# Performance work log

Measured on AMD Instinct MI355X. Metric: run time of the kernel, lower is better.

Reference implementation:

```python
import jax, jax.numpy as jnp
import numpy as np

B, S_SRC, S_TRG = 128, 512, 128
VIN, VOUT = 128, 128
E, H = 128, 256          # embed, encoder hidden
HD = 2 * H               # decoder hidden = 512 (concat of bi-dir encoder states)
DENC = 2 * H             # encoder output feature dim = 512


def setup_inputs() -> dict:
    key = jax.random.key(0)
    ks = jax.random.split(key, 20)
    g = lambda k, shape: (jax.random.normal(k, shape, jnp.float32) * 0.05)
    inp = {
        "src": jax.random.randint(ks[0], (B, S_SRC), 0, VIN, jnp.int32),
        "trg": jax.random.randint(ks[1], (B, S_TRG), 0, VOUT, jnp.int32),
        # encoder
        "enc_emb": g(ks[2], (VIN, E)),
        "enc_Wih_f": g(ks[3], (4 * H, E)),
        "enc_Whh_f": g(ks[4], (4 * H, H)),
        "enc_b_f": g(ks[5], (4 * H,)),
        "enc_Wih_b": g(ks[6], (4 * H, E)),
        "enc_Whh_b": g(ks[7], (4 * H, H)),
        "enc_b_b": g(ks[8], (4 * H,)),
        # decoder
        "dec_emb": g(ks[9], (VOUT, E)),
        "dec_Wih": g(ks[10], (4 * HD, E + DENC)),
        "dec_Whh": g(ks[11], (4 * HD, HD)),
        "dec_b": g(ks[12], (4 * HD,)),
        # attention: Linear(dec_hid + enc_dim -> HD), v: Linear(HD -> 1)
        "attn_W": g(ks[13], (HD + DENC, HD)),
        "attn_b": g(ks[14], (HD,)),
        "attn_v": g(ks[15], (HD,)),
        # output projection
        "out_W": g(ks[16], (HD, VOUT)),
        "out_b": g(ks[17], (VOUT,)),
    }
    return inp


def _lstm_cell(h, c, x, Wih, Whh, b):
    gates = x @ Wih.T + h @ Whh.T + b               # [B, 4H]
    i, f, gg, o = jnp.split(gates, 4, axis=-1)       # PyTorch gate order i,f,g,o
    i, f, o = jax.nn.sigmoid(i), jax.nn.sigmoid(f), jax.nn.sigmoid(o)
    c = f * c + i * jnp.tanh(gg)
    h = o * jnp.tanh(c)
    return h, c


def _lstm_scan(xs, Wih, Whh, b, reverse=False):
    # xs: [S, B, E] -> hs: [S, B, H] (time-aligned), plus final (h, c)
    Bn, Hn = xs.shape[1], Whh.shape[1]
    init = (jnp.zeros((Bn, Hn), xs.dtype), jnp.zeros((Bn, Hn), xs.dtype))
    def step(carry, x):
        h, c = _lstm_cell(carry[0], carry[1], x, Wih, Whh, b)
        return (h, c), h
    (h, c), hs = jax.lax.scan(step, init, xs, reverse=reverse)
    return hs, h, c


def reference(src, trg, enc_emb, enc_Wih_f, enc_Whh_f, enc_b_f,
              enc_Wih_b, enc_Whh_b, enc_b_b, dec_emb, dec_Wih, dec_Whh,
              dec_b, attn_W, attn_b, attn_v, out_W, out_b):
    # ----- encoder (bidirectional LSTM) -----
    emb = enc_emb[src]                                # [B, S, E]
    xs = jnp.swapaxes(emb, 0, 1)                      # [S, B, E]
    hs_f, hf, cf = _lstm_scan(xs, enc_Wih_f, enc_Whh_f, enc_b_f, reverse=False)
    hs_b, hb, cb = _lstm_scan(xs, enc_Wih_b, enc_Whh_b, enc_b_b, reverse=True)
    enc_out = jnp.swapaxes(jnp.concatenate([hs_f, hs_b], -1), 0, 1)  # [B, S, 2H]
    hidden = jnp.concatenate([hf, hb], -1)            # [B, HD]  (hidden.view(1,B,-1))
    cell = jnp.concatenate([cf, cb], -1)              # [B, HD]

    # attention linear split: energy = tanh([h, enc] @ W + b)
    Wh, We = attn_W[:HD], attn_W[HD:]
    enc_proj = jnp.einsum("bsd,de->bse", enc_out, We)  # [B, S, HD] precomputed

    def dec_step(carry, tok):
        h, c = carry
        e = jnp.tanh(h[:, None, :] @ Wh + enc_proj + attn_b)     # [B, S, HD]
        scores = jnp.einsum("bse,e->bs", e, attn_v)              # [B, S]
        aw = jax.nn.softmax(scores, axis=1)
        ctx = jnp.einsum("bs,bsd->bd", aw, enc_out)              # [B, DENC]
        x = jnp.concatenate([dec_emb[tok], ctx], -1)             # [B, E+DENC]
        h, c = _lstm_cell(h, c, x, dec_Wih, dec_Whh, dec_b)
        logits = h @ out_W + out_b                               # [B, VOUT]
        return (h, c), logits

    # teacher forcing (ratio=1.0): input at step t is trg[:, t-1], t = 1..T-1
    toks = jnp.swapaxes(trg[:, :-1], 0, 1)            # [T-1, B]
    _, logits = jax.lax.scan(dec_step, (hidden, cell), toks)
    logits = jnp.swapaxes(logits, 0, 1)               # [B, T-1, VOUT]
    outputs = jnp.concatenate(
        [jnp.zeros((src.shape[0], 1, VOUT), logits.dtype), logits], axis=1)
    return outputs
```

## Files before the change

kernel.cpp:

```cpp
#include <hip/hip_runtime.h>


typedef _Float16 f16;
typedef _Float16 half8 __attribute__((ext_vector_type(8)));
typedef float f32x4 __attribute__((ext_vector_type(4)));
typedef char char8v __attribute__((ext_vector_type(8)));

#define MFMA16(a, b, c) __builtin_amdgcn_mfma_f32_16x16x32_f16((a), (b), (c), 0, 0, 0)

#define PSCALE (2.5f / 127.f)
#define PINV   (127.f / 2.5f)

__device__ __forceinline__ float fsig(float x) {
    return __builtin_amdgcn_rcpf(1.f + __expf(-x));
}
__device__ __forceinline__ float ftanh(float x) {
    return 1.f - 2.f * __builtin_amdgcn_rcpf(1.f + __expf(2.f * x));
}
__device__ __forceinline__ int frag_idx(int m, int k, int KS) {
    return (((m >> 4) * KS + (k >> 5)) * 64 + (((k >> 3) & 3) * 16 + (m & 15))) * 8 + (k & 7);
}

__device__ __forceinline__ void lds_barrier() {
    asm volatile("s_waitcnt lgkmcnt(0)" ::: "memory");
    __builtin_amdgcn_sched_barrier(0);
    __builtin_amdgcn_s_barrier();
    __builtin_amdgcn_sched_barrier(0);
}

__global__ void k_zero(unsigned* __restrict__ s)
{
    for (int z = threadIdx.x; z < 4112; z += 256) s[z] = 0u;
}

__global__ __launch_bounds__(256) void k_prep(
    const float* __restrict__ attn_W, const float* __restrict__ out_W,
    const float* __restrict__ enc_emb,
    const float* __restrict__ wihf, const float* __restrict__ wihb,
    const float* __restrict__ whhf, const float* __restrict__ whhb,
    const float* __restrict__ dec_emb, const float* __restrict__ dec_wih,
    const float* __restrict__ dec_whh,
    f16* __restrict__ WhT_sw, f16* __restrict__ outWT_sw,
    f16* __restrict__ whhf_sw, f16* __restrict__ whhb_sw,
    f16* __restrict__ decwih_sw, f16* __restrict__ decwhh_sw,
    f16* __restrict__ WeT, f16* __restrict__ emb16,
    f16* __restrict__ wihf16, f16* __restrict__ wihb16,
    f16* __restrict__ decemb16, float* __restrict__ out)
{
    long i = (long)blockIdx.x * 256 + threadIdx.x;
    if (i >= 3784704L) return;
    long idx = i;
    if (idx < 262144) {
        int j = idx & 7, lane = (idx >> 3) & 63, c = lane & 15, q = lane >> 4;
        int ks = (idx >> 9) & 15, nt = idx >> 13;
        WhT_sw[idx] = (f16)attn_W[(ks * 32 + q * 8 + j) * 512 + nt * 16 + c];
        return;
    }
    idx -= 262144;
    if (idx < 65536) {
        int j = idx & 7, lane = (idx >> 3) & 63, c = lane & 15, q = lane >> 4;
        int ks = (idx >> 9) & 15, nt = idx >> 13;
        outWT_sw[idx] = (f16)out_W[(ks * 32 + q * 8 + j) * 128 + nt * 16 + c];
        return;
    }
    idx -= 65536;
    if (idx < 262144) {
        int j = idx & 7, lane = (idx >> 3) & 63, c = lane & 15, q = lane >> 4;
        int ks = (idx >> 9) & 7, nt = idx >> 12;
        whhf_sw[idx] = (f16)whhf[(nt * 16 + c) * 256 + ks * 32 + q * 8 + j];
        return;
    }
    idx -= 262144;
    if (idx < 262144) {
        int j = idx & 7, lane = (idx >> 3) & 63, c = lane & 15, q = lane >> 4;
        int ks = (idx >> 9) & 7, nt = idx >> 12;
        whhb_sw[idx] = (f16)whhb[(nt * 16 + c) * 256 + ks * 32 + q * 8 + j];
        return;
    }
    idx -= 262144;
    if (idx < 1310720) {
        int j = idx & 7, lane = (idx >> 3) & 63, c = lane & 15, q = lane >> 4;
        int r2 = idx >> 9; int ks = r2 % 20, nt = r2 / 20;
        decwih_sw[idx] = (f16)dec_wih[(nt * 16 + c) * 640 + ks * 32 + q * 8 + j];
        return;
    }
    idx -= 1310720;
    if (idx < 1048576) {
        int j = idx & 7, lane = (idx >> 3) & 63, c = lane & 15, q = lane >> 4;
        int ks = (idx >> 9) & 15, nt = idx >> 13;
        decwhh_sw[idx] = (f16)dec_whh[(nt * 16 + c) * 512 + ks * 32 + q * 8 + j];
        return;
    }
    idx -= 1048576;
    if (idx < 262144) { int e = idx >> 9, d = idx & 511; WeT[idx] = (f16)attn_W[(512 + d) * 512 + e]; return; }
    idx -= 262144;
    if (idx < 16384)  { emb16[idx] = (f16)enc_emb[idx]; return; }
    idx -= 16384;
    if (idx < 131072) { wihf16[idx] = (f16)wihf[idx]; return; }
    idx -= 131072;
    if (idx < 131072) { wihb16[idx] = (f16)wihb[idx]; return; }
    idx -= 131072;
    if (idx < 16384)  { decemb16[idx] = (f16)dec_emb[idx]; return; }
    idx -= 16384;
    if (idx < 16384)  { int b = idx >> 7, v = idx & 127; out[b * 16384 + v] = 0.f; return; }
}

__global__ __launch_bounds__(256) void k_vocab(
    const f16* __restrict__ emb, const f16* __restrict__ wihf,
    const f16* __restrict__ wihb, const float* __restrict__ bf_,
    const float* __restrict__ bb_, f16* __restrict__ xg_vocab)
{
    int bn = blockIdx.x;
    int tid = threadIdx.x, wave = tid >> 6, lane = tid & 63;
    int col = lane & 15, quad = lane >> 4;
    int wr = wave >> 1, wc = wave & 1;

    f32x4 acc[4][4] = {};
    for (int ks = 0; ks < 4; ++ks) {
        int k0 = ks * 32 + quad * 8;
        half8 a[4], bfr[4];
        for (int i = 0; i < 4; ++i)
            a[i] = *(const half8*)(emb + (wr * 64 + i * 16 + col) * 128 + k0);
        for (int j = 0; j < 4; ++j) {
            int n = bn * 128 + wc * 64 + j * 16 + col;
            const f16* wp = (n < 1024) ? (wihf + n * 128) : (wihb + (n - 1024) * 128);
            bfr[j] = *(const half8*)(wp + k0);
        }
        for (int i = 0; i < 4; ++i)
            for (int j = 0; j < 4; ++j)
                acc[i][j] = MFMA16(a[i], bfr[j], acc[i][j]);
    }
    for (int j = 0; j < 4; ++j) {
        int n = bn * 128 + wc * 64 + j * 16 + col;
        float bias = (n < 1024) ? bf_[n] : bb_[n - 1024];
        for (int i = 0; i < 4; ++i) {
            int vbase = wr * 64 + i * 16 + quad * 4;
            for (int r = 0; r < 4; ++r)
                xg_vocab[(vbase + r) * 2048 + n] = (f16)(acc[i][j][r] + bias);
        }
    }
}

__global__ __launch_bounds__(512, 1) void k_enc(
    const int* __restrict__ src, const f16* __restrict__ xg_vocab,
    const f16* __restrict__ whhf_sw, const f16* __restrict__ whhb_sw,
    f16* __restrict__ enc_out, f16* __restrict__ hdec0, float* __restrict__ c_ws)
{
    int blk = blockIdx.x;
    int dir = blk >> 3, bbase = (blk & 7) * 16;
    int tid = threadIdx.x, wave = tid >> 6, lane = tid & 63;
    int col = lane & 15, quad = lane >> 4;
    const f16* whh = dir ? whhb_sw : whhf_sw;

    __shared__ f16 hb[2][16][264];
    __shared__ f16 xvb[2][16][1032];
    __shared__ unsigned short stall[8192];

    for (int z = tid; z < 2 * 16 * 264; z += 512) ((f16*)hb)[z] = (f16)0.f;
    for (int z = tid; z < 8192; z += 512) stall[z] = (unsigned short)src[bbase * 512 + z];
    float cc[2][4] = {};

    half8 bst[16];
    #pragma unroll
    for (int nt = 0; nt < 2; ++nt)
        #pragma unroll
        for (int kk = 0; kk < 8; ++kk) {
            int tile = wave * 2 + nt;
            bst[nt * 8 + kk] = *(const half8*)(whh + ((tile * 8 + kk) * 64 + lane) * 8);
        }
    __syncthreads();

    int xrow = tid >> 7, xoff = (tid & 127) * 8;
    half8 xr[4];
    {
        int ts0 = dir ? 511 : 0;
        #pragma unroll
        for (int it = 0; it < 4; ++it) {
            int row = it * 4 + xrow;
            int tok = stall[row * 512 + ts0];
            xr[it] = *(const half8*)(xg_vocab + tok * 2048 + dir * 1024 + xoff);
        }
        #pragma unroll
        for (int it = 0; it < 4; ++it)
            *(half8*)(&xvb[0][it * 4 + xrow][xoff]) = xr[it];
    }
    __syncthreads();

    int ts_prev = 0;
    for (int t = 0; t < 512; ++t) {
        int ts = dir ? (511 - t) : t;
        int cur = t & 1, prv = cur ^ 1;

        if (t < 511) {
            int tsn = dir ? (510 - t) : (t + 1);
            #pragma unroll
            for (int it = 0; it < 4; ++it) {
                int row = it * 4 + xrow;
                int tok = stall[row * 512 + tsn];
                xr[it] = *(const half8*)(xg_vocab + tok * 2048 + dir * 1024 + xoff);
            }
        }

        if (t > 0) {
            int b = tid >> 5, seg = tid & 31;
            *(half8*)(enc_out + ((size_t)(bbase + b) * 512 + ts_prev) * 512 + dir * 256 + seg * 8) =
                *(const half8*)(&hb[prv][b][seg * 8]);
        }

        half8 a[8];
        #pragma unroll
        for (int kk = 0; kk < 8; ++kk)
            a[kk] = *(const half8*)(&hb[prv][col][kk * 32 + quad * 8]);

        f32x4 acc[4][2] = {};
        #pragma unroll
        for (int kk = 0; kk < 8; ++kk) {
            half8 bv[6];
            #pragma unroll
            for (int g = 1; g < 4; ++g)
                #pragma unroll
                for (int nt = 0; nt < 2; ++nt) {
                    int tile = g * 16 + wave * 2 + nt;
                    bv[(g - 1) * 2 + nt] =
                        *(const half8*)(whh + ((tile * 8 + kk) * 64 + lane) * 8);
                }
            #pragma unroll
            for (int nt = 0; nt < 2; ++nt)
                acc[0][nt] = MFMA16(a[kk], bst[nt * 8 + kk], acc[0][nt]);
            #pragma unroll
            for (int g = 1; g < 4; ++g)
                #pragma unroll
                for (int nt = 0; nt < 2; ++nt)
                    acc[g][nt] = MFMA16(a[kk], bv[(g - 1) * 2 + nt], acc[g][nt]);
        }

        #pragma unroll
        for (int nt = 0; nt < 2; ++nt) {
            int hcol = wave * 32 + nt * 16 + col;
            #pragma unroll
            for (int r = 0; r < 4; ++r) {
                int b = quad * 4 + r;
                float gi = (float)xvb[cur][b][0 * 256 + hcol] + acc[0][nt][r];
                float gf = (float)xvb[cur][b][1 * 256 + hcol] + acc[1][nt][r];
                float gg = (float)xvb[cur][b][2 * 256 + hcol] + acc[2][nt][r];
                float go = (float)xvb[cur][b][3 * 256 + hcol] + acc[3][nt][r];
                float ig = fsig(gi), fg = fsig(gf), g2 = ftanh(gg), og = fsig(go);
                float cv = fg * cc[nt][r] + ig * g2;
                cc[nt][r] = cv;
                float h = og * ftanh(cv);
                hb[cur][b][hcol] = (f16)h;
            }
        }

        if (t < 511) {
            #pragma unroll
            for (int it = 0; it < 4; ++it)
                *(half8*)(&xvb[prv][it * 4 + xrow][xoff]) = xr[it];
        }

        lds_barrier();
        ts_prev = ts;
    }

    {
        int b = tid >> 5, seg = tid & 31;
        *(half8*)(enc_out + ((size_t)(bbase + b) * 512 + ts_prev) * 512 + dir * 256 + seg * 8) =
            *(const half8*)(&hb[1][b][seg * 8]);
    }
    #pragma unroll
    for (int nt = 0; nt < 2; ++nt) {
        int hcol = wave * 32 + nt * 16 + col;
        #pragma unroll
        for (int r = 0; r < 4; ++r) {
            int b = quad * 4 + r;
            int m = bbase + b, k = dir * 256 + hcol;
            hdec0[frag_idx(m, k, 16)] = hb[1][b][hcol];
            c_ws[m * 512 + k] = cc[nt][r];
        }
    }
}

__global__ __launch_bounds__(256) void k_proj(
    const f16* __restrict__ enc_out, const f16* __restrict__ WeT,
    char* __restrict__ proj8)
{
    int blk = blockIdx.x;
    int bm = blk & 511, bn = blk >> 9;
    int tid = threadIdx.x, wave = tid >> 6, lane = tid & 63;
    int col = lane & 15, quad = lane >> 4;
    int wr = wave >> 1, wc = wave & 1;

    f32x4 acc[4][4] = {};
    for (int ks = 0; ks < 16; ++ks) {
        int k0 = ks * 32 + quad * 8;
        half8 a[4], bfr[4];
        for (int i = 0; i < 4; ++i) {
            int m = bm * 128 + wr * 64 + i * 16 + col;
            a[i] = *(const half8*)(enc_out + (size_t)m * 512 + k0);
        }
        for (int j = 0; j < 4; ++j) {
            int n = bn * 128 + wc * 64 + j * 16 + col;
            bfr[j] = *(const half8*)(WeT + n * 512 + k0);
        }
        for (int i = 0; i < 4; ++i)
            for (int j = 0; j < 4; ++j)
                acc[i][j] = MFMA16(a[i], bfr[j], acc[i][j]);
    }
    for (int j = 0; j < 4; ++j) {
        int n = bn * 128 + wc * 64 + j * 16 + col;
        for (int i = 0; i < 4; ++i) {
            int mbase = bm * 128 + wr * 64 + i * 16 + quad * 4;
            for (int r = 0; r < 4; ++r) {
                float v = acc[i][j][r] * PINV;
                int q = (int)rintf(v);
                q = (q > 127) ? 127 : ((q < -127) ? -127 : q);
                proj8[(size_t)(mbase + r) * 512 + n] = (char)q;
            }
        }
    }
}

__global__ __launch_bounds__(256) void k_qinit(
    const f16* __restrict__ h0_sw, const f16* __restrict__ WhT_sw,
    float* __restrict__ qpart)
{
    int j = blockIdx.x;
    int tid = threadIdx.x, wave = tid >> 6, lane = tid & 63;
    int col = lane & 15, quad = lane >> 4;
    half8 a[2];
    #pragma unroll
    for (int i = 0; i < 2; ++i)
        a[i] = *(const half8*)(h0_sw + (((wave * 2 + i) * 16 + j) * 64 + lane) * 8);
    for (int nt = 0; nt < 32; ++nt) {
        half8 bfr = *(const half8*)(WhT_sw + ((nt * 16 + j) * 64 + lane) * 8);
        f32x4 q0 = {}, q1 = {};
        q0 = MFMA16(a[0], bfr, q0);
        q1 = MFMA16(a[1], bfr, q1);
        #pragma unroll
        for (int r = 0; r < 4; ++r) {
            qpart[(j * 128 + wave * 32 + quad * 4 + r) * 512 + nt * 16 + col] = q0[r];
            qpart[(j * 128 + wave * 32 + 16 + quad * 4 + r) * 512 + nt * 16 + col] = q1[r];
        }
    }
}

__global__ __launch_bounds__(512, 4) void k_step(
    const char* __restrict__ proj8, const f16* __restrict__ enc_out,
    float* __restrict__ qpart, const float* __restrict__ attn_bp,
    const float* __restrict__ attn_vp, const int* __restrict__ trg,
    const f16* __restrict__ dec_emb, f16* __restrict__ x_sw,
    float* __restrict__ part_m, float* __restrict__ part_l,
    float* __restrict__ part_ctx, f16* __restrict__ hdec0,
    f16* __restrict__ hdec1, const f16* __restrict__ wih_sw,
    const f16* __restrict__ whh_sw, const float* __restrict__ dec_bp,
    float* __restrict__ c_ws, f16* __restrict__ hhist_sw,
    const f16* __restrict__ WhT_sw, unsigned* __restrict__ flags, int tt)
{
    int blk = blockIdx.x;
    int tid = threadIdx.x, wave = tid >> 6, lane = tid & 63;
    int col = lane & 15, quad = lane >> 4;

    __shared__ float q[512];
    __shared__ float sc[256];
    __shared__ float ctxred[8][512];
    __shared__ float wred[8], wred2[8];
    __shared__ f16 hsl[64][40];
    __shared__ float gm[64][2];

    if (blk < 32) {
        int tg = tt - 1;
        if (tg >= 0) {
            int j = blk >> 1, mh = blk & 1;
            if (tid < 64) {
                int bb = mh * 64 + tid;
                float m0 = part_m[bb * 2 + 0], m1 = part_m[bb * 2 + 1];
                float l0 = part_l[bb * 2 + 0], l1 = part_l[bb * 2 + 1];
                float M = fmaxf(m0, m1);
                float g0 = __expf(m0 - M), g1 = __expf(m1 - M);
                float inv = 1.f / (g0 * l0 + g1 * l1);
                gm[tid][0] = g0 * inv;
                gm[tid][1] = g1 * inv;
            }
            __syncthreads();
            for (int z = tid; z < 32768; z += 512) {
                int lr = z >> 9, d = z & 511;
                int bb = mh * 64 + lr;
                float c = gm[lr][0] * part_ctx[(size_t)(bb * 2 + 0) * 512 + d]
                        + gm[lr][1] * part_ctx[(size_t)(bb * 2 + 1) * 512 + d];
                x_sw[frag_idx(bb, 128 + d, 20)] = (f16)c;
            }
            __syncthreads();

            if (tid < 256) {
                const f16* hprev = (tg & 1) ? hdec1 : hdec0;
                f16* hnext = (tg & 1) ? hdec0 : hdec1;

                f32x4 acc[8] = {};
                for (int ks = 0; ks < 36; ++ks) {
                    int mtile = mh * 4 + wave;
                    half8 a = (ks < 20)
                        ? *(const half8*)(x_sw + ((mtile * 20 + ks) * 64 + lane) * 8)
                        : *(const half8*)(hprev + ((mtile * 16 + (ks - 20)) * 64 + lane) * 8);
                    half8 bv[8];
                    #pragma unroll
                    for (int jt = 0; jt < 8; ++jt) {
                        int g = jt >> 1, u2 = jt & 1;
                        int ntile = g * 32 + j * 2 + u2;
                        bv[jt] = (ks < 20)
                            ? *(const half8*)(wih_sw + ((ntile * 20 + ks) * 64 + lane) * 8)
                            : *(const half8*)(whh_sw + ((ntile * 16 + (ks - 20)) * 64 + lane) * 8);
                    }
                    #pragma unroll
                    for (int jt = 0; jt < 8; ++jt)
                        acc[jt] = MFMA16(a, bv[jt], acc[jt]);
                }
                float bias[8];
                #pragma unroll
                for (int jt = 0; jt < 8; ++jt) {
                    int g = jt >> 1, u2 = jt & 1;
                    bias[jt] = dec_bp[g * 512 + j * 32 + u2 * 16 + col];
                }
                #pragma unroll
                for (int r = 0; r < 4; ++r) {
                    int lb = wave * 16 + quad * 4 + r;
                    int bb = mh * 64 + lb;
                    #pragma unroll
                    for (int u2 = 0; u2 < 2; ++u2) {
                        int hl = u2 * 16 + col, hcol = j * 32 + hl;
                        float gi = acc[0 + u2][r] + bias[0 + u2];
                        float gf = acc[2 + u2][r] + bias[2 + u2];
                        float gg = acc[4 + u2][r] + bias[4 + u2];
                        float go = acc[6 + u2][r] + bias[6 + u2];
                        float ig = fsig(gi), fg = fsig(gf), g2 = ftanh(gg), og = fsig(go);
                        float cv = fg * c_ws[bb * 512 + hcol] + ig * g2;
                        c_ws[bb * 512 + hcol] = cv;
                        float h = og * ftanh(cv);
                        f16 h16 = (f16)h;
                        int fidx = frag_idx(bb, hcol, 16);
                        hnext[fidx] = h16;
                        hhist_sw[tg * 65536 + fidx] = h16;
                        hsl[lb][hl] = h16;
                    }
                }
                half8 aq = *(const half8*)(&hsl[wave * 16 + col][quad * 8]);
                for (int nt = 0; nt < 32; ++nt) {
                    half8 bq = *(const half8*)(WhT_sw + ((nt * 16 + j) * 64 + lane) * 8);
                    f32x4 q0 = {};
                    q0 = MFMA16(aq, bq, q0);
                    #pragma unroll
                    for (int r = 0; r < 4; ++r)
                        qpart[(j * 128 + mh * 64 + wave * 16 + quad * 4 + r) * 512 + nt * 16 + col] = q0[r];
                }
            }

            __syncthreads();
            if (tid == 0)
                __hip_atomic_store(flags + blk * 16, (unsigned)tt,
                                   __ATOMIC_RELEASE, __HIP_MEMORY_SCOPE_AGENT);
        }
        return;
    }

    int ab = blk - 32;
    int b = ab >> 1, sh = ab & 1;
    int sbase = sh * 256;

    float vreg[8];
    #pragma unroll
    for (int u = 0; u < 8; ++u) vreg[u] = attn_vp[lane * 8 + u];
    float abias = attn_bp[tid];

    char8v p0[8];
    #pragma unroll
    for (int z = 0; z < 8; ++z) {
        int sl = z * 8 + wave;
        p0[z] = *(const char8v*)(proj8 + ((size_t)b * 512 + sbase + sl) * 512 + lane * 8);
    }

    if (tt > 0) {
        if (wave == 0) {
            for (;;) {
                unsigned v = (lane < 32)
                    ? __hip_atomic_load(flags + lane * 16, __ATOMIC_RELAXED,
                                        __HIP_MEMORY_SCOPE_AGENT)
                    : (unsigned)tt;
                if (__ballot(v >= (unsigned)tt) == ~0ull) break;
                __builtin_amdgcn_s_sleep(8);
            }
            if (lane == 0)
                (void)__hip_atomic_load(flags, __ATOMIC_ACQUIRE,
                                        __HIP_MEMORY_SCOPE_AGENT);
        }
        __syncthreads();
    }

    {
        float s = abias;
        #pragma unroll
        for (int jj = 0; jj < 16; ++jj) s += qpart[(jj * 128 + b) * 512 + tid];
        q[tid] = s;
    }
    __syncthreads();

    float qreg[8];
    #pragma unroll
    for (int u = 0; u < 8; ++u) qreg[u] = q[lane * 8 + u];

    #pragma unroll
    for (int z = 0; z < 8; ++z) {
        int sl = z * 8 + wave;
        float part = 0.f;
        #pragma unroll
        for (int u = 0; u < 8; ++u)
            part += vreg[u] * ftanh(fmaf((float)p0[z][u], PSCALE, qreg[u]));
        #pragma unroll
        for (int o = 32; o; o >>= 1) part += __shfl_xor(part, o);
        if (lane == 0) sc[sl] = part;
    }
    for (int ib = 1; ib < 4; ++ib) {
        char8v p[8];
        #pragma unroll
        for (int z = 0; z < 8; ++z) {
            int sl = (ib * 8 + z) * 8 + wave;
            p[z] = *(const char8v*)(proj8 + ((size_t)b * 512 + sbase + sl) * 512 + lane * 8);
        }
        #pragma unroll
        for (int z = 0; z < 8; ++z) {
            int sl = (ib * 8 + z) * 8 + wave;
            float part = 0.f;
            #pragma unroll
            for (int u = 0; u < 8; ++u)
                part += vreg[u] * ftanh(fmaf((float)p[z][u], PSCALE, qreg[u]));
            #pragma unroll
            for (int o = 32; o; o >>= 1) part += __shfl_xor(part, o);
            if (lane == 0) sc[sl] = part;
        }
    }
    __syncthreads();

    float s0 = (tid < 256) ? sc[tid] : -__builtin_inff();
    float mv = s0;
    #pragma unroll
    for (int o = 32; o; o >>= 1) mv = fmaxf(mv, __shfl_xor(mv, o));
    if (lane == 0) wred[wave] = mv;
    __syncthreads();
    float M = wred[0];
    #pragma unroll
    for (int w = 1; w < 8; ++w) M = fmaxf(M, wred[w]);
    float e0 = (tid < 256) ? __expf(s0 - M) : 0.f;
    if (tid < 256) sc[tid] = e0;
    float sm = e0;
    #pragma unroll
    for (int o = 32; o; o >>= 1) sm += __shfl_xor(sm, o);
    if (lane == 0) wred2[wave] = sm;
    __syncthreads();
    float lsum = wred2[0];
    #pragma unroll
    for (int w = 1; w < 8; ++w) lsum += wred2[w];

    float a8[8] = {};
    for (int ib = 0; ib < 4; ++ib) {
        half8 ev[8];
        float wgt[8];
        #pragma unroll
        for (int z = 0; z < 8; ++z) {
            int sl = (ib * 8 + z) * 8 + wave;
            ev[z] = *(const half8*)(enc_out + ((size_t)b * 512 + sbase + sl) * 512 + lane * 8);
            wgt[z] = sc[sl];
        }
        #pragma unroll
        for (int z = 0; z < 8; ++z)
            #pragma unroll
            for (int u = 0; u < 8; ++u) a8[u] += wgt[z] * (float)ev[z][u];
    }
    #pragma unroll
    for (int u = 0; u < 8; ++u) ctxred[wave][lane * 8 + u] = a8[u];
    __syncthreads();
    float cp = 0.f;
    #pragma unroll
    for (int w = 0; w < 8; ++w) cp += ctxred[w][tid];
    part_ctx[(size_t)ab * 512 + tid] = cp;
    if (tid == 0) { part_m[ab] = M; part_l[ab] = lsum; }

    if (sh == 0 && tid < 128) {
        int tok = trg[b * 128 + tt];
        x_sw[frag_idx(b, tid, 20)] = dec_emb[tok * 128 + tid];
    }
}

__global__ __launch_bounds__(256) void k_gates(
    f16* __restrict__ x_sw, const f16* __restrict__ hprev_sw,
    const f16* __restrict__ wih_sw, const f16* __restrict__ whh_sw,
    const float* __restrict__ dec_b, float* __restrict__ c_ws,
    f16* __restrict__ hnext_sw, f16* __restrict__ hhist_sw,
    const f16* __restrict__ WhT_sw, float* __restrict__ qpart,
    const float* __restrict__ part_m, const float* __restrict__ part_l,
    const float* __restrict__ part_ctx, int t)
{
    int jb = blockIdx.x;
    int j = jb >> 1, mh = jb & 1;
    int tid = threadIdx.x, wave = tid >> 6, lane = tid & 63;
    int col = lane & 15, quad = lane >> 4;
    __shared__ f16 hsl[64][40];
    __shared__ float gm[64][2];

    if (tid < 64) {
        int bb = mh * 64 + tid;
        float m0 = part_m[bb * 2 + 0], m1 = part_m[bb * 2 + 1];
        float l0 = part_l[bb * 2 + 0], l1 = part_l[bb * 2 + 1];
        float M = fmaxf(m0, m1);
        float g0 = __expf(m0 - M), g1 = __expf(m1 - M);
        float inv = 1.f / (g0 * l0 + g1 * l1);
        gm[tid][0] = g0 * inv;
        gm[tid][1] = g1 * inv;
    }
    __syncthreads();
    for (int z = tid; z < 32768; z += 256) {
        int lr = z >> 9, d = z & 511;
        int bb = mh * 64 + lr;
        float c = gm[lr][0] * part_ctx[(size_t)(bb * 2 + 0) * 512 + d]
                + gm[lr][1] * part_ctx[(size_t)(bb * 2 + 1) * 512 + d];
        x_sw[frag_idx(bb, 128 + d, 20)] = (f16)c;
    }
    __syncthreads();

    f32x4 acc[8] = {};
    for (int ks = 0; ks < 36; ++ks) {
        int mtile = mh * 4 + wave;
        half8 a = (ks < 20)
            ? *(const half8*)(x_sw + ((mtile * 20 + ks) * 64 + lane) * 8)
            : *(const half8*)(hprev_sw + ((mtile * 16 + (ks - 20)) * 64 + lane) * 8);
        half8 bv[8];
        #pragma unroll
        for (int jt = 0; jt < 8; ++jt) {
            int g = jt >> 1, u2 = jt & 1;
            int ntile = g * 32 + j * 2 + u2;
            bv[jt] = (ks < 20)
                ? *(const half8*)(wih_sw + ((ntile * 20 + ks) * 64 + lane) * 8)
                : *(const half8*)(whh_sw + ((ntile * 16 + (ks - 20)) * 64 + lane) * 8);
        }
        #pragma unroll
        for (int jt = 0; jt < 8; ++jt)
            acc[jt] = MFMA16(a, bv[jt], acc[jt]);
    }
    float bias[8];
    #pragma unroll
    for (int jt = 0; jt < 8; ++jt) {
        int g = jt >> 1, u2 = jt & 1;
        bias[jt] = dec_b[g * 512 + j * 32 + u2 * 16 + col];
    }
    #pragma unroll
    for (int r = 0; r < 4; ++r) {
        int lb = wave * 16 + quad * 4 + r;
        int bb = mh * 64 + lb;
        #pragma unroll
        for (int u2 = 0; u2 < 2; ++u2) {
            int hl = u2 * 16 + col, hcol = j * 32 + hl;
            float gi = acc[0 + u2][r] + bias[0 + u2];
            float gf = acc[2 + u2][r] + bias[2 + u2];
            float gg = acc[4 + u2][r] + bias[4 + u2];
            float go = acc[6 + u2][r] + bias[6 + u2];
            float ig = fsig(gi), fg = fsig(gf), g2 = ftanh(gg), og = fsig(go);
            float cv = fg * c_ws[bb * 512 + hcol] + ig * g2;
            c_ws[bb * 512 + hcol] = cv;
            float h = og * ftanh(cv);
            f16 h16 = (f16)h;
            int fidx = frag_idx(bb, hcol, 16);
            hnext_sw[fidx] = h16;
            hhist_sw[t * 65536 + fidx] = h16;
            hsl[lb][hl] = h16;
        }
    }
    half8 aq = *(const half8*)(&hsl[wave * 16 + col][quad * 8]);
    for (int nt = 0; nt < 32; ++nt) {
        half8 bq = *(const half8*)(WhT_sw + ((nt * 16 + j) * 64 + lane) * 8);
        f32x4 q0 = {};
        q0 = MFMA16(aq, bq, q0);
        #pragma unroll
        for (int r = 0; r < 4; ++r)
            qpart[(j * 128 + mh * 64 + wave * 16 + quad * 4 + r) * 512 + nt * 16 + col] = q0[r];
    }
}

__global__ __launch_bounds__(256) void k_logits(
    const f16* __restrict__ hhist_sw, const f16* __restrict__ outWT_sw,
    const float* __restrict__ out_b, float* __restrict__ out)
{
    int bt = blockIdx.x;
    int tid = threadIdx.x, wave = tid >> 6, lane = tid & 63;
    int col = lane & 15, quad = lane >> 4;
    f32x4 acc[2][8] = {};
    for (int ks = 0; ks < 16; ++ks) {
        half8 a[2];
        #pragma unroll
        for (int i = 0; i < 2; ++i)
            a[i] = *(const half8*)(hhist_sw + bt * 65536 + (((wave * 2 + i) * 16 + ks) * 64 + lane) * 8);
        half8 bv[8];
        #pragma unroll
        for (int jt = 0; jt < 8; ++jt)
            bv[jt] = *(const half8*)(outWT_sw + ((jt * 16 + ks) * 64 + lane) * 8);
        #pragma unroll
        for (int jt = 0; jt < 8; ++jt) {
            acc[0][jt] = MFMA16(a[0], bv[jt], acc[0][jt]);
            acc[1][jt] = MFMA16(a[1], bv[jt], acc[1][jt]);
        }
    }
    #pragma unroll
    for (int jt = 0; jt < 8; ++jt) {
        float bias = out_b[jt * 16 + col];
        #pragma unroll
        for (int i = 0; i < 2; ++i)
            #pragma unroll
            for (int r = 0; r < 4; ++r) {
                int br = wave * 32 + i * 16 + quad * 4 + r;
                out[br * 16384 + (bt + 1) * 128 + jt * 16 + col] = acc[i][jt][r] + bias;
            }
    }
}

extern "C" void kernel_launch(void* const* d_in, const int* in_sizes, int n_in,
                              void* d_out, int out_size, void* d_ws, size_t ws_size,
                              hipStream_t stream)
{
    (void)in_sizes; (void)n_in; (void)out_size;
    if (ws_size < 130000000) return;

    const int*   src     = (const int*)d_in[0];
    const int*   trg     = (const int*)d_in[1];
    const float* enc_emb = (const float*)d_in[2];
    const float* wihf    = (const float*)d_in[3];
    const float* whhf    = (const float*)d_in[4];
    const float* bf_     = (const float*)d_in[5];
    const float* wihb    = (const float*)d_in[6];
    const float* whhb    = (const float*)d_in[7];
    const float* bb_     = (const float*)d_in[8];
    const float* dec_emb = (const float*)d_in[9];
    const float* dec_wih = (const float*)d_in[10];
    const float* dec_whh = (const float*)d_in[11];
    const float* dec_b   = (const float*)d_in[12];
    const float* attn_W  = (const float*)d_in[13];
    const float* attn_b  = (const float*)d_in[14];
    const float* attn_v  = (const float*)d_in[15];
    const float* out_W   = (const float*)d_in[16];
    const float* out_b   = (const float*)d_in[17];
    float* out = (float*)d_out;

    char* p = (char*)d_ws;
    auto carve = [&](size_t n) { char* r = p; p += ((n + 255) & ~(size_t)255); return r; };
    f16*   enc_out   = (f16*)  carve(67108864);
    char*  proj8     = (char*) carve(33554432);
    f16*   WhT_sw    = (f16*)  carve(524288);
    f16*   WeT       = (f16*)  carve(524288);
    f16*   outWT_sw  = (f16*)  carve(131072);
    f16*   emb16     = (f16*)  carve(32768);
    f16*   wihf16    = (f16*)  carve(262144);
    f16*   wihb16    = (f16*)  carve(262144);
    f16*   whhf_sw   = (f16*)  carve(524288);
    f16*   whhb_sw   = (f16*)  carve(524288);
    f16*   decemb16  = (f16*)  carve(32768);
    f16*   decwih_sw = (f16*)  carve(2621440);
    f16*   decwhh_sw = (f16*)  carve(2097152);
    float* qpart     = (float*)carve(4194304);
    f16*   hdec0     = (f16*)  carve(131072);
    f16*   hdec1     = (f16*)  carve(131072);
    float* c_ws      = (float*)carve(262144);
    f16*   x_sw      = (f16*)  carve(163840);
    f16*   hhist_sw  = (f16*)  carve(16646144);
    f16*   xg_vocab  = (f16*)  carve(524288);
    float* part_m    = (float*)carve(2048);
    float* part_l    = (float*)carve(2048);
    float* part_ctx  = (float*)carve(524288);
    unsigned* flagsv = (unsigned*)carve(16448);

    k_zero<<<1, 256, 0, stream>>>(flagsv);
    k_prep<<<14784, 256, 0, stream>>>(attn_W, out_W, enc_emb, wihf, wihb, whhf, whhb,
                                      dec_emb, dec_wih, dec_whh,
                                      WhT_sw, outWT_sw, whhf_sw, whhb_sw,
                                      decwih_sw, decwhh_sw, WeT, emb16,
                                      wihf16, wihb16, decemb16, out);
    k_vocab<<<16, 256, 0, stream>>>(emb16, wihf16, wihb16, bf_, bb_, xg_vocab);
    k_enc<<<16, 512, 0, stream>>>(src, xg_vocab, whhf_sw, whhb_sw, enc_out, hdec0, c_ws);
    k_proj<<<2048, 256, 0, stream>>>(enc_out, WeT, proj8);
    k_qinit<<<16, 256, 0, stream>>>(hdec0, WhT_sw, qpart);

    for (int tt = 0; tt < 127; ++tt)
        k_step<<<288, 512, 0, stream>>>(proj8, enc_out, qpart, attn_b, attn_v,
                                        trg, decemb16, x_sw, part_m, part_l,
                                        part_ctx, hdec0, hdec1, decwih_sw,
                                        decwhh_sw, dec_b, c_ws, hhist_sw,
                                        WhT_sw, flagsv, tt);
    k_gates<<<32, 256, 0, stream>>>(x_sw, hdec0, decwih_sw, decwhh_sw, dec_b,
                                    c_ws, hdec1, hhist_sw, WhT_sw, qpart,
                                    part_m, part_l, part_ctx, 126);

    k_logits<<<127, 256, 0, stream>>>(hhist_sw, outWT_sw, out_b, out);
}
```

Measured before the change: 12.52 ms.

## Split decoder LSTM gate GEMM across all eight waves and batch loads

The decoder LSTM blocks now use all 8 waves instead of 4. Each wave pair splits the gate columns: half the waves compute i/f gates and the other half g/o, exchanging results through a new shared buffer. The q-projection tail is also split across wave halves. Loads are batched in groups of four k-steps to expose memory-level parallelism, and the context combine is restructured so each thread handles one feature column. Launch bounds drop to 2 blocks per CU, which may lower occupancy, and the change adds an extra barrier and LDS traffic.

```diff
diff --git a/kernel.cpp b/kernel.cpp
--- a/kernel.cpp
+++ b/kernel.cpp
@@ -344,7 +344,7 @@
     }
 }
 
-__global__ __launch_bounds__(512, 4) void k_step(
+__global__ __launch_bounds__(512, 2) void k_step(
     const char* __restrict__ proj8, const f16* __restrict__ enc_out,
     float* __restrict__ qpart, const float* __restrict__ attn_bp,
     const float* __restrict__ attn_vp, const int* __restrict__ trg,
@@ -366,6 +366,7 @@
     __shared__ float wred[8], wred2[8];
     __shared__ f16 hsl[64][40];
     __shared__ float gm[64][2];
+    __shared__ float gq[4][4][4][64];
 
     if (blk < 32) {
         int tg = tt - 1;
@@ -382,74 +383,127 @@
                 gm[tid][1] = g1 * inv;
             }
             __syncthreads();
-            for (int z = tid; z < 32768; z += 512) {
-                int lr = z >> 9, d = z & 511;
-                int bb = mh * 64 + lr;
-                float c = gm[lr][0] * part_ctx[(size_t)(bb * 2 + 0) * 512 + d]
-                        + gm[lr][1] * part_ctx[(size_t)(bb * 2 + 1) * 512 + d];
-                x_sw[frag_idx(bb, 128 + d, 20)] = (f16)c;
+
+            for (int io = 0; io < 64; io += 8) {
+                float p0[8], p1[8];
+                #pragma unroll
+                for (int k = 0; k < 8; ++k) {
+                    int bb = mh * 64 + io + k;
+                    p0[k] = part_ctx[(size_t)(bb * 2 + 0) * 512 + tid];
+                    p1[k] = part_ctx[(size_t)(bb * 2 + 1) * 512 + tid];
+                }
+                #pragma unroll
+                for (int k = 0; k < 8; ++k) {
+                    int lr = io + k, bb = mh * 64 + lr;
+                    x_sw[frag_idx(bb, 128 + tid, 20)] =
+                        (f16)(gm[lr][0] * p0[k] + gm[lr][1] * p1[k]);
+                }
             }
             __syncthreads();
 
-            if (tid < 256) {
-                const f16* hprev = (tg & 1) ? hdec1 : hdec0;
-                f16* hnext = (tg & 1) ? hdec0 : hdec1;
-
-                f32x4 acc[8] = {};
-                for (int ks = 0; ks < 36; ++ks) {
-                    int mtile = mh * 4 + wave;
-                    half8 a = (ks < 20)
-                        ? *(const half8*)(x_sw + ((mtile * 20 + ks) * 64 + lane) * 8)
-                        : *(const half8*)(hprev + ((mtile * 16 + (ks - 20)) * 64 + lane) * 8);
-                    half8 bv[8];
+            const f16* hprev = (tg & 1) ? hdec1 : hdec0;
+            f16* hnext = (tg & 1) ? hdec0 : hdec1;
+
+            int h = wave >> 2, mw = wave & 3;
+            int mtile = mh * 4 + mw;
+
+            f32x4 acc[4] = {};
+            for (int kg = 0; kg < 20; kg += 4) {
+                half8 ag[4], bvg[4][4];
+                #pragma unroll
+                for (int kk = 0; kk < 4; ++kk) {
+                    int ks = kg + kk;
+                    ag[kk] = *(const half8*)(x_sw + ((mtile * 20 + ks) * 64 + lane) * 8);
                     #pragma unroll
-                    for (int jt = 0; jt < 8; ++jt) {
-                        int g = jt >> 1, u2 = jt & 1;
+                    for (int q2 = 0; q2 < 4; ++q2) {
+                        int jt = h * 4 + q2, g = jt >> 1, u2 = jt & 1;
                         int ntile = g * 32 + j * 2 + u2;
-                        bv[jt] = (ks < 20)
-                            ? *(const half8*)(wih_sw + ((ntile * 20 + ks) * 64 + lane) * 8)
-                            : *(const half8*)(whh_sw + ((ntile * 16 + (ks - 20)) * 64 + lane) * 8);
+                        bvg[kk][q2] = *(const half8*)(wih_sw + ((ntile * 20 + ks) * 64 + lane) * 8);
                     }
+                }
+                #pragma unroll
+                for (int kk = 0; kk < 4; ++kk)
                     #pragma unroll
-                    for (int jt = 0; jt < 8; ++jt)
-                        acc[jt] = MFMA16(a, bv[jt], acc[jt]);
+                    for (int q2 = 0; q2 < 4; ++q2)
+                        acc[q2] = MFMA16(ag[kk], bvg[kk][q2], acc[q2]);
+            }
+            for (int kg = 0; kg < 16; kg += 4) {
+                half8 ag[4], bvg[4][4];
+                #pragma unroll
+                for (int kk = 0; kk < 4; ++kk) {
+                    int ks2 = kg + kk;
+                    ag[kk] = *(const half8*)(hprev + ((mtile * 16 + ks2) * 64 + lane) * 8);
+                    #pragma unroll
+                    for (int q2 = 0; q2 < 4; ++q2) {
+                        int jt = h * 4 + q2, g = jt >> 1, u2 = jt & 1;
+                        int ntile = g * 32 + j * 2 + u2;
+                        bvg[kk][q2] = *(const half8*)(whh_sw + ((ntile * 16 + ks2) * 64 + lane) * 8);
+                    }
                 }
-                float bias[8];
-                #pragma unroll
-                for (int jt = 0; jt < 8; ++jt) {
-                    int g = jt >> 1, u2 = jt & 1;
-                    bias[jt] = dec_bp[g * 512 + j * 32 + u2 * 16 + col];
-                }
+                #pragma unroll
+                for (int kk = 0; kk < 4; ++kk)
+                    #pragma unroll
+                    for (int q2 = 0; q2 < 4; ++q2)
+                        acc[q2] = MFMA16(ag[kk], bvg[kk][q2], acc[q2]);
+            }
+
+            float bias[4];
+            #pragma unroll
+            for (int q2 = 0; q2 < 4; ++q2) {
+                int jt = h * 4 + q2, g = jt >> 1, u2 = jt & 1;
+                bias[q2] = dec_bp[g * 512 + j * 32 + u2 * 16 + col];
+            }
+            if (h == 1) {
+                #pragma unroll
+                for (int q2 = 0; q2 < 4; ++q2)
+                    #pragma unroll
+                    for (int r = 0; r < 4; ++r)
+                        gq[mw][q2][r][lane] = acc[q2][r] + bias[q2];
+            }
+            __syncthreads();
+
+            if (h == 0) {
                 #pragma unroll
                 for (int r = 0; r < 4; ++r) {
-                    int lb = wave * 16 + quad * 4 + r;
+                    int lb = mw * 16 + quad * 4 + r;
                     int bb = mh * 64 + lb;
                     #pragma unroll
                     for (int u2 = 0; u2 < 2; ++u2) {
                         int hl = u2 * 16 + col, hcol = j * 32 + hl;
                         float gi = acc[0 + u2][r] + bias[0 + u2];
                         float gf = acc[2 + u2][r] + bias[2 + u2];
-                        float gg = acc[4 + u2][r] + bias[4 + u2];
-                        float go = acc[6 + u2][r] + bias[6 + u2];
+                        float gg = gq[mw][0 + u2][r][lane];
+                        float go = gq[mw][2 + u2][r][lane];
                         float ig = fsig(gi), fg = fsig(gf), g2 = ftanh(gg), og = fsig(go);
                         float cv = fg * c_ws[bb * 512 + hcol] + ig * g2;
                         c_ws[bb * 512 + hcol] = cv;
-                        float h = og * ftanh(cv);
-                        f16 h16 = (f16)h;
+                        float hv = og * ftanh(cv);
+                        f16 h16 = (f16)hv;
                         int fidx = frag_idx(bb, hcol, 16);
                         hnext[fidx] = h16;
                         hhist_sw[tg * 65536 + fidx] = h16;
                         hsl[lb][hl] = h16;
                     }
                 }
-                half8 aq = *(const half8*)(&hsl[wave * 16 + col][quad * 8]);
-                for (int nt = 0; nt < 32; ++nt) {
-                    half8 bq = *(const half8*)(WhT_sw + ((nt * 16 + j) * 64 + lane) * 8);
+            }
+            __syncthreads();
+
+            half8 aq = *(const half8*)(&hsl[mw * 16 + col][quad * 8]);
+            for (int ng = 0; ng < 4; ++ng) {
+                half8 bq[4];
+                #pragma unroll
+                for (int k = 0; k < 4; ++k) {
+                    int nt = h * 16 + ng * 4 + k;
+                    bq[k] = *(const half8*)(WhT_sw + ((nt * 16 + j) * 64 + lane) * 8);
+                }
+                #pragma unroll
+                for (int k = 0; k < 4; ++k) {
+                    int nt = h * 16 + ng * 4 + k;
                     f32x4 q0 = {};
-                    q0 = MFMA16(aq, bq, q0);
+                    q0 = MFMA16(aq, bq[k], q0);
                     #pragma unroll
                     for (int r = 0; r < 4; ++r)
-                        qpart[(j * 128 + mh * 64 + wave * 16 + quad * 4 + r) * 512 + nt * 16 + col] = q0[r];
+                        qpart[(j * 128 + mh * 64 + mw * 16 + quad * 4 + r) * 512 + nt * 16 + col] = q0[r];
                 }
             }
 
```

Result: faster. 10.94 ms (-12.6%).
